# Performance work log

Measured on AMD Instinct MI355X. Metric: run time of the kernel, lower is better.

The kernel has to match this reference:

```python
import jax, jax.numpy as jnp
import numpy as np

B, C_IN, H, W = 8, 32, 64, 64
C = 64  # num_channels


def setup_inputs() -> dict:
    key = jax.random.key(0)
    ks = jax.random.split(key, 9)
    s_in = 1.0 / np.sqrt(C_IN)
    s_c = 1.0 / np.sqrt(C)
    return {
        "x": jax.random.normal(ks[0], (B, C_IN, H, W), dtype=jnp.float32),
        "wq": jax.random.uniform(ks[1], (C, C_IN), jnp.float32, -s_in, s_in),
        "bq": jax.random.uniform(ks[2], (C,), jnp.float32, -s_in, s_in),
        "wk": jax.random.uniform(ks[3], (C, C_IN), jnp.float32, -s_in, s_in),
        "bk": jax.random.uniform(ks[4], (C,), jnp.float32, -s_in, s_in),
        "wv": jax.random.uniform(ks[5], (C, C_IN), jnp.float32, -s_in, s_in),
        "bv": jax.random.uniform(ks[6], (C,), jnp.float32, -s_in, s_in),
        "wo": jax.random.uniform(ks[7], (C_IN, C), jnp.float32, -s_c, s_c),
        "bo": jax.random.uniform(ks[8], (C_IN,), jnp.float32, -s_c, s_c),
    }


def reference(x, wq, bq, wk, bk, wv, bv, wo, bo):
    b, c_in, h, w = x.shape
    n = h * w
    # 1x1 convs == per-pixel linear projections; produce (B, N, C) directly
    q = (jnp.einsum('bchw,oc->bhwo', x, wq) + bq).reshape(b, n, -1)
    k = (jnp.einsum('bchw,oc->bhwo', x, wk) + bk).reshape(b, n, -1)
    v = (jnp.einsum('bchw,oc->bhwo', x, wv) + bv).reshape(b, n, -1)
    # unscaled attention over spatial positions (no 1/sqrt(d) in original)
    scores = jnp.einsum('bnc,bmc->bnm', q, k)  # (B, N, N)
    attn = jax.nn.softmax(scores, axis=-1)
    out = jnp.einsum('bnm,bmc->bnc', attn, v)  # (B, N, C)
    out = out.reshape(b, h, w, -1)
    out = jnp.einsum('bhwc,oc->bohw', out, wo) + bo[None, :, None, None]
    return out + x
```

## Files before the change

### kernel.cpp

```cpp
#include <hip/hip_runtime.h>
#include <hip/hip_bf16.h>

#define CIN    32
#define NPIX   4096
#define DIM    64
#define LOG2E  1.4426950408889634f

#if __has_builtin(__builtin_amdgcn_exp2f)
#define EXP2(x) __builtin_amdgcn_exp2f(x)
#else
#define EXP2(x) exp2f(x)
#endif

typedef float  f32x4  __attribute__((ext_vector_type(4)));
typedef float  f32x16 __attribute__((ext_vector_type(16)));
typedef short  s16x8  __attribute__((ext_vector_type(8)));

#define ZERO16 {0.f,0.f,0.f,0.f,0.f,0.f,0.f,0.f,0.f,0.f,0.f,0.f,0.f,0.f,0.f,0.f}

__device__ __forceinline__ f32x16 mfma32(s16x8 a, s16x8 b, f32x16 c) {
    return __builtin_amdgcn_mfma_f32_32x32x16_bf16(a, b, c, 0, 0, 0);
}


__global__ __launch_bounds__(256) void qkv_proj(
    const float* __restrict__ x,
    const float* __restrict__ wq, const float* __restrict__ bq,
    const float* __restrict__ wk, const float* __restrict__ bk,
    const float* __restrict__ wv, const float* __restrict__ bv,
    __hip_bfloat16* __restrict__ qb, __hip_bfloat16* __restrict__ kb,
    __hip_bfloat16* __restrict__ vb)
{
    __shared__ float Xs[CIN][64];
    __shared__ float wT[3][CIN][DIM];

    const int tid = threadIdx.x;
    const int b   = blockIdx.y;
    const int bx  = blockIdx.x;
    const int n0  = bx * 64;

    for (int i = tid; i < 3 * CIN * DIM; i += 256) {
        int m = i >> 11, r = i & 2047, c = r >> 6, o = r & 63;
        const float* wsrc = (m == 0) ? wq : (m == 1) ? wk : wv;
        float wv0 = wsrc[o * CIN + c];
        wT[m][c][o] = (m == 0) ? wv0 * LOG2E : wv0;
    }
    for (int i = tid * 4; i < CIN * 64; i += 1024) {
        int c = i >> 6, p = i & 63;
        *(f32x4*)&Xs[c][p] = *(const f32x4*)&x[((size_t)b * CIN + c) * NPIX + n0 + p];
    }
    __syncthreads();

    const int w    = tid >> 6;
    const int lane = tid & 63;
    const int l16  = lane >> 2;
    const int quad = lane & 3;

    const int T  = bx * 4 + w;
    const int px = T * 16 + l16;

    float aq[2][8], ak[2][8];
    #pragma unroll
    for (int kb2 = 0; kb2 < 2; kb2++) {
        f32x4 bq0 = *(const f32x4*)&bq[kb2 * 32 + quad * 8];
        f32x4 bq1 = *(const f32x4*)&bq[kb2 * 32 + quad * 8 + 4];
        f32x4 bk0 = *(const f32x4*)&bk[kb2 * 32 + quad * 8];
        f32x4 bk1 = *(const f32x4*)&bk[kb2 * 32 + quad * 8 + 4];
        #pragma unroll
        for (int j = 0; j < 4; j++) {
            aq[kb2][j] = bq0[j] * LOG2E; aq[kb2][j + 4] = bq1[j] * LOG2E;
            ak[kb2][j] = bk0[j];         ak[kb2][j + 4] = bk1[j];
        }
    }
    #pragma unroll 8
    for (int c = 0; c < CIN; c++) {
        const float xc = Xs[c][w * 16 + l16];
        #pragma unroll
        for (int kb2 = 0; kb2 < 2; kb2++) {
            f32x4 q0 = *(const f32x4*)&wT[0][c][kb2 * 32 + quad * 8];
            f32x4 q1 = *(const f32x4*)&wT[0][c][kb2 * 32 + quad * 8 + 4];
            f32x4 k0 = *(const f32x4*)&wT[1][c][kb2 * 32 + quad * 8];
            f32x4 k1 = *(const f32x4*)&wT[1][c][kb2 * 32 + quad * 8 + 4];
            #pragma unroll
            for (int j = 0; j < 4; j++) {
                aq[kb2][j]     += xc * q0[j];
                aq[kb2][j + 4] += xc * q1[j];
                ak[kb2][j]     += xc * k0[j];
                ak[kb2][j + 4] += xc * k1[j];
            }
        }
    }
    {
        const int s   = px >> 5;
        const int key = px & 31;
        #pragma unroll
        for (int kb2 = 0; kb2 < 2; kb2++) {
            union { s16x8 v; __hip_bfloat16 h[8]; } pq, pk;
            #pragma unroll
            for (int j = 0; j < 8; j++) {
                pq.h[j] = __float2bfloat16(aq[kb2][j]);
                pk.h[j] = __float2bfloat16(ak[kb2][j]);
            }
            *(s16x8*)(qb + ((size_t)b * NPIX + px) * DIM + kb2 * 32 + quad * 8) = pq.v;
            const int kt = kb2 * 2 + (quad >> 1);
            const int h  = quad & 1;
            const size_t koff = (size_t)b * 262144
                + ((size_t)(s * 4 + kt) * 64 + h * 32 + key) * 8;
            *(s16x8*)(kb + koff) = pk.v;
        }
    }

    const int ch = w * 16 + l16;
    float av[2][8];
    {
        const float bvc = bv[ch];
        #pragma unroll
        for (int kh = 0; kh < 2; kh++)
            #pragma unroll
            for (int j = 0; j < 8; j++) av[kh][j] = bvc;
    }
    #pragma unroll 8
    for (int c = 0; c < CIN; c++) {
        const float wvc = wT[2][c][ch];
        f32x4 x0 = *(const f32x4*)&Xs[c][quad * 8];
        f32x4 x1 = *(const f32x4*)&Xs[c][quad * 8 + 4];
        f32x4 x2 = *(const f32x4*)&Xs[c][32 + quad * 8];
        f32x4 x3 = *(const f32x4*)&Xs[c][32 + quad * 8 + 4];
        #pragma unroll
        for (int j = 0; j < 4; j++) {
            av[0][j]     += x0[j] * wvc;
            av[0][j + 4] += x1[j] * wvc;
            av[1][j]     += x2[j] * wvc;
            av[1][j + 4] += x3[j] * wvc;
        }
    }
    #pragma unroll
    for (int kh = 0; kh < 2; kh++) {
        const int s = bx * 2 + kh;
        #pragma unroll
        for (int h = 0; h < 2; h++) {
            union { unsigned long long u; __hip_bfloat16 hh[4]; } pv;
            #pragma unroll
            for (int j = 0; j < 4; j++) pv.hh[j] = __float2bfloat16(av[kh][h * 4 + j]);
            const size_t voff = (size_t)b * 262144
                + (size_t)(s * 4 + (ch >> 5) * 2 + (quad >> 1)) * 512
                + (size_t)(h * 32 + (ch & 31)) * 8
                + 4 * (quad & 1);
            *(unsigned long long*)(vb + voff) = pv.u;
        }
    }
}

__global__ __launch_bounds__(512, 2) void attn_fused(
    const __hip_bfloat16* __restrict__ qb,
    const __hip_bfloat16* __restrict__ kbf,
    const __hip_bfloat16* __restrict__ vbf,
    const float* __restrict__ wo, const float* __restrict__ bo,
    const float* __restrict__ x, float* __restrict__ y)
{
    __shared__ __align__(16) char  sm[2][8][4096];
    __shared__ __align__(16) float REDx[4][64][33];
    __shared__ float LRED2[4][32];

    const int tid  = threadIdx.x;
    const int w    = tid >> 6;
    const int g    = w >> 1;
    const int h    = w & 1;
    const int lane = tid & 63;
    const int q    = lane & 31;
    const int hl   = lane >> 5;
    const int b    = blockIdx.x;
    const int row0 = blockIdx.y * 128 + g * 32;

    s16x8 qf[4];
    #pragma unroll
    for (int kt = 0; kt < 4; kt++)
        qf[kt] = *(const s16x8*)(qb + ((size_t)b * NPIX + row0 + q) * DIM
                                 + kt * 16 + hl * 8);

    f32x16 o0 = ZERO16, o1 = ZERO16;
    float lsacc = 0.f;

    const char* stbase = ((w >> 2) ? (const char*)vbf : (const char*)kbf)
                       + (size_t)b * 524288
                       + (size_t)((w >> 1) & 1) * 262144
                       + (size_t)(w & 1) * 4096
                       + (size_t)lane * 16;
    char* std0 = &sm[0][w][lane * 16];
    char* std1 = &sm[1][w][lane * 16];

    #pragma unroll
    for (int i = 0; i < 4; i++)
        *(f32x4*)(std0 + i * 1024) = *(const f32x4*)(stbase + i * 1024);
    __syncthreads();

    int cur = 0;
    for (int p = 0; p < 32; ++p) {
        const size_t srcoff = (size_t)((p < 31) ? p + 1 : 31) * 8192;
        f32x4 r0 = *(const f32x4*)(stbase + srcoff);
        f32x4 r1 = *(const f32x4*)(stbase + srcoff + 1024);
        f32x4 r2 = *(const f32x4*)(stbase + srcoff + 2048);
        f32x4 r3 = *(const f32x4*)(stbase + srcoff + 3072);

        const char* K0 = sm[cur][h * 2 + 0];
        const char* K1 = sm[cur][h * 2 + 1];
        const char* V0 = sm[cur][4 + h * 2 + 0];
        const char* V1 = sm[cur][4 + h * 2 + 1];
        s16x8 kf0[4], kf1[4], vv0[4], vv1[4];
        #pragma unroll
        for (int i = 0; i < 4; i++) {
            kf0[i] = *(const s16x8*)(K0 + i * 1024 + lane * 16);
            kf1[i] = *(const s16x8*)(K1 + i * 1024 + lane * 16);
            vv0[i] = *(const s16x8*)(V0 + i * 1024 + lane * 16);
            vv1[i] = *(const s16x8*)(V1 + i * 1024 + lane * 16);
        }

        __builtin_amdgcn_s_setprio(1);
        f32x16 s0 = ZERO16, s1 = ZERO16;
        s0 = mfma32(kf0[0], qf[0], s0);
        s1 = mfma32(kf1[0], qf[0], s1);
        s0 = mfma32(kf0[1], qf[1], s0);
        s1 = mfma32(kf1[1], qf[1], s1);
        s0 = mfma32(kf0[2], qf[2], s0);
        s1 = mfma32(kf1[2], qf[2], s1);
        s0 = mfma32(kf0[3], qf[3], s0);
        s1 = mfma32(kf1[3], qf[3], s1);
        __builtin_amdgcn_s_setprio(0);

        union { s16x8 v; __hip_bfloat16 h8[8]; } p00, p01, p10, p11;
        #pragma unroll
        for (int r = 0; r < 16; r++) { s0[r] = EXP2(s0[r]); lsacc += s0[r]; }
        #pragma unroll
        for (int j = 0; j < 8; j++) {
            p00.h8[j] = __float2bfloat16(s0[j]);
            p01.h8[j] = __float2bfloat16(s0[8 + j]);
        }
        #pragma unroll
        for (int r = 0; r < 16; r++) { s1[r] = EXP2(s1[r]); lsacc += s1[r]; }
        #pragma unroll
        for (int j = 0; j < 8; j++) {
            p10.h8[j] = __float2bfloat16(s1[j]);
            p11.h8[j] = __float2bfloat16(s1[8 + j]);
        }

        __builtin_amdgcn_s_setprio(1);
        o0 = mfma32(vv0[0], p00.v, o0);
        o1 = mfma32(vv0[2], p00.v, o1);
        o0 = mfma32(vv0[1], p01.v, o0);
        o1 = mfma32(vv0[3], p01.v, o1);
        o0 = mfma32(vv1[0], p10.v, o0);
        o1 = mfma32(vv1[2], p10.v, o1);
        o0 = mfma32(vv1[1], p11.v, o0);
        o1 = mfma32(vv1[3], p11.v, o1);
        __builtin_amdgcn_s_setprio(0);

        char* dst = cur ? std0 : std1;
        *(f32x4*)(dst)        = r0;
        *(f32x4*)(dst + 1024) = r1;
        *(f32x4*)(dst + 2048) = r2;
        *(f32x4*)(dst + 3072) = r3;
        __syncthreads();
        cur ^= 1;
    }

    lsacc += __shfl_xor(lsacc, 32, 64);

    if (h == 1) {
        #pragma unroll
        for (int i = 0; i < 16; i++) {
            const int rr = (i & 3) + 8 * (i >> 2) + 4 * hl;
            REDx[g][rr][q]      = o0[i];
            REDx[g][32 + rr][q] = o1[i];
        }
        if (hl == 0) LRED2[g][q] = lsacc;
    }
    __syncthreads();

    if (h == 0) {
        const float lsum = lsacc + LRED2[g][q];
        #pragma unroll
        for (int i = 0; i < 16; i++) {
            const int rr = (i & 3) + 8 * (i >> 2) + 4 * hl;
            o0[i] += REDx[g][rr][q];
            o1[i] += REDx[g][32 + rr][q];
        }
        const float inv = 1.0f / lsum;

        s16x8 pbo[4];
        #pragma unroll
        for (int gg = 0; gg < 4; gg++) {
            union { s16x8 v; __hip_bfloat16 h8[8]; } pk;
            #pragma unroll
            for (int j = 0; j < 8; j++) {
                const float vv = (gg < 2) ? o0[(gg & 1) * 8 + j] : o1[(gg & 1) * 8 + j];
                pk.h8[j] = __float2bfloat16(vv * inv);
            }
            pbo[gg] = pk.v;
        }

        s16x8 aw[4];
        #pragma unroll
        for (int gg = 0; gg < 4; gg++) {
            f32x4 w0 = *(const f32x4*)(wo + (size_t)q * DIM + gg * 16 + hl * 4);
            f32x4 w1 = *(const f32x4*)(wo + (size_t)q * DIM + gg * 16 + 8 + hl * 4);
            union { s16x8 v; __hip_bfloat16 h8[8]; } wf;
            #pragma unroll
            for (int j = 0; j < 4; j++) {
                wf.h8[j]     = __float2bfloat16(w0[j]);
                wf.h8[4 + j] = __float2bfloat16(w1[j]);
            }
            aw[gg] = wf.v;
        }

        f32x16 d = ZERO16;
        #pragma unroll
        for (int gg = 0; gg < 4; gg++)
            d = mfma32(aw[gg], pbo[gg], d);

        #pragma unroll
        for (int i = 0; i < 16; i++) {
            const int out = (i & 3) + 8 * (i >> 2) + 4 * hl;
            const int row = row0 + q;
            const size_t xi = ((size_t)b * CIN + out) * NPIX + row;
            y[xi] = d[i] + bo[out] + x[xi];
        }
    }
}

extern "C" void kernel_launch(void* const* d_in, const int* in_sizes, int n_in,
                              void* d_out, int out_size, void* d_ws, size_t ws_size,
                              hipStream_t stream)
{
    const float* x  = (const float*)d_in[0];
    const float* wq = (const float*)d_in[1];
    const float* bq = (const float*)d_in[2];
    const float* wk = (const float*)d_in[3];
    const float* bk = (const float*)d_in[4];
    const float* wv = (const float*)d_in[5];
    const float* bv = (const float*)d_in[6];
    const float* wo = (const float*)d_in[7];
    const float* bo = (const float*)d_in[8];
    float* y = (float*)d_out;

    char* ws = (char*)d_ws;
    __hip_bfloat16* qb = (__hip_bfloat16*)(ws);
    __hip_bfloat16* kb = (__hip_bfloat16*)(ws + (4u << 20));
    __hip_bfloat16* vb = (__hip_bfloat16*)(ws + (8u << 20));

    qkv_proj<<<dim3(64, 8), dim3(256), 0, stream>>>(x, wq, bq, wk, bk, wv, bv, qb, kb, vb);
    attn_fused<<<dim3(8, 32), dim3(512), 0, stream>>>(qb, kb, vb, wo, bo, x, y);
}
```

Measured before the change: 127.6 us.

## Software-pipeline PV MFMAs one tile behind QK and exp in attention loop

```diff
diff --git a/kernel.cpp b/kernel.cpp
--- a/kernel.cpp
+++ b/kernel.cpp
@@ -194,25 +194,40 @@
         *(f32x4*)(std0 + i * 1024) = *(const f32x4*)(stbase + i * 1024);
     __syncthreads();
 
-    int cur = 0;
-    for (int p = 0; p < 32; ++p) {
+    s16x8 vvA[8], vvB[8], pA[4], pB[4];
+
+    auto phase = [&](int p, int cur,
+                     s16x8 (&vvP)[8], s16x8 (&pP)[4],
+                     s16x8 (&vvO)[8], s16x8 (&pO)[4], bool do_pv) {
+        const char* K0 = sm[cur][h * 2 + 0];
+        const char* K1 = sm[cur][h * 2 + 1];
+        const char* V0 = sm[cur][4 + h * 2 + 0];
+        const char* V1 = sm[cur][4 + h * 2 + 1];
+        s16x8 kf0[4], kf1[4];
+        #pragma unroll
+        for (int i = 0; i < 4; i++) {
+            kf0[i]     = *(const s16x8*)(K0 + i * 1024 + lane * 16);
+            kf1[i]     = *(const s16x8*)(K1 + i * 1024 + lane * 16);
+            vvO[i]     = *(const s16x8*)(V0 + i * 1024 + lane * 16);
+            vvO[4 + i] = *(const s16x8*)(V1 + i * 1024 + lane * 16);
+        }
         const size_t srcoff = (size_t)((p < 31) ? p + 1 : 31) * 8192;
         f32x4 r0 = *(const f32x4*)(stbase + srcoff);
         f32x4 r1 = *(const f32x4*)(stbase + srcoff + 1024);
         f32x4 r2 = *(const f32x4*)(stbase + srcoff + 2048);
         f32x4 r3 = *(const f32x4*)(stbase + srcoff + 3072);
 
-        const char* K0 = sm[cur][h * 2 + 0];
-        const char* K1 = sm[cur][h * 2 + 1];
-        const char* V0 = sm[cur][4 + h * 2 + 0];
-        const char* V1 = sm[cur][4 + h * 2 + 1];
-        s16x8 kf0[4], kf1[4], vv0[4], vv1[4];
-        #pragma unroll
-        for (int i = 0; i < 4; i++) {
-            kf0[i] = *(const s16x8*)(K0 + i * 1024 + lane * 16);
-            kf1[i] = *(const s16x8*)(K1 + i * 1024 + lane * 16);
-            vv0[i] = *(const s16x8*)(V0 + i * 1024 + lane * 16);
-            vv1[i] = *(const s16x8*)(V1 + i * 1024 + lane * 16);
+        if (do_pv) {
+            __builtin_amdgcn_s_setprio(1);
+            o0 = mfma32(vvP[0], pP[0], o0);
+            o1 = mfma32(vvP[2], pP[0], o1);
+            o0 = mfma32(vvP[1], pP[1], o0);
+            o1 = mfma32(vvP[3], pP[1], o1);
+            o0 = mfma32(vvP[4], pP[2], o0);
+            o1 = mfma32(vvP[6], pP[2], o1);
+            o0 = mfma32(vvP[5], pP[3], o0);
+            o1 = mfma32(vvP[7], pP[3], o1);
+            __builtin_amdgcn_s_setprio(0);
         }
 
         __builtin_amdgcn_s_setprio(1);
@@ -227,32 +242,24 @@
         s1 = mfma32(kf1[3], qf[3], s1);
         __builtin_amdgcn_s_setprio(0);
 
-        union { s16x8 v; __hip_bfloat16 h8[8]; } p00, p01, p10, p11;
-        #pragma unroll
-        for (int r = 0; r < 16; r++) { s0[r] = EXP2(s0[r]); lsacc += s0[r]; }
+        union { s16x8 v; __hip_bfloat16 h8[8]; } u0, u1, u2, u3;
         #pragma unroll
         for (int j = 0; j < 8; j++) {
-            p00.h8[j] = __float2bfloat16(s0[j]);
-            p01.h8[j] = __float2bfloat16(s0[8 + j]);
-        }
-        #pragma unroll
-        for (int r = 0; r < 16; r++) { s1[r] = EXP2(s1[r]); lsacc += s1[r]; }
+            float e0 = EXP2(s0[j]);
+            float e1 = EXP2(s0[8 + j]);
+            lsacc += e0 + e1;
+            u0.h8[j] = __float2bfloat16(e0);
+            u1.h8[j] = __float2bfloat16(e1);
+        }
         #pragma unroll
         for (int j = 0; j < 8; j++) {
-            p10.h8[j] = __float2bfloat16(s1[j]);
-            p11.h8[j] = __float2bfloat16(s1[8 + j]);
-        }
-
-        __builtin_amdgcn_s_setprio(1);
-        o0 = mfma32(vv0[0], p00.v, o0);
-        o1 = mfma32(vv0[2], p00.v, o1);
-        o0 = mfma32(vv0[1], p01.v, o0);
-        o1 = mfma32(vv0[3], p01.v, o1);
-        o0 = mfma32(vv1[0], p10.v, o0);
-        o1 = mfma32(vv1[2], p10.v, o1);
-        o0 = mfma32(vv1[1], p11.v, o0);
-        o1 = mfma32(vv1[3], p11.v, o1);
-        __builtin_amdgcn_s_setprio(0);
+            float e0 = EXP2(s1[j]);
+            float e1 = EXP2(s1[8 + j]);
+            lsacc += e0 + e1;
+            u2.h8[j] = __float2bfloat16(e0);
+            u3.h8[j] = __float2bfloat16(e1);
+        }
+        pO[0] = u0.v; pO[1] = u1.v; pO[2] = u2.v; pO[3] = u3.v;
 
         char* dst = cur ? std0 : std1;
         *(f32x4*)(dst)        = r0;
@@ -260,8 +267,24 @@
         *(f32x4*)(dst + 2048) = r2;
         *(f32x4*)(dst + 3072) = r3;
         __syncthreads();
-        cur ^= 1;
-    }
+    };
+
+    phase(0, 0, vvB, pB, vvA, pA, false);
+    for (int it = 0; it < 15; ++it) {
+        phase(2 * it + 1, 1, vvA, pA, vvB, pB, true);
+        phase(2 * it + 2, 0, vvB, pB, vvA, pA, true);
+    }
+    phase(31, 1, vvA, pA, vvB, pB, true);
+    __builtin_amdgcn_s_setprio(1);
+    o0 = mfma32(vvB[0], pB[0], o0);
+    o1 = mfma32(vvB[2], pB[0], o1);
+    o0 = mfma32(vvB[1], pB[1], o0);
+    o1 = mfma32(vvB[3], pB[1], o1);
+    o0 = mfma32(vvB[4], pB[2], o0);
+    o1 = mfma32(vvB[6], pB[2], o1);
+    o0 = mfma32(vvB[5], pB[3], o0);
+    o1 = mfma32(vvB[7], pB[3], o1);
+    __builtin_amdgcn_s_setprio(0);
 
     lsacc += __shfl_xor(lsacc, 32, 64);
 
@@ -292,8 +315,8 @@
             union { s16x8 v; __hip_bfloat16 h8[8]; } pk;
             #pragma unroll
             for (int j = 0; j < 8; j++) {
-                const float vv = (gg < 2) ? o0[(gg & 1) * 8 + j] : o1[(gg & 1) * 8 + j];
-                pk.h8[j] = __float2bfloat16(vv * inv);
+                const float vv2 = (gg < 2) ? o0[(gg & 1) * 8 + j] : o1[(gg & 1) * 8 + j];
+                pk.h8[j] = __float2bfloat16(vv2 * inv);
             }
             pbo[gg] = pk.v;
         }
```

After: 127.0 us. Within noise of the previous version (-0.5%).

## Compute QKV projection with split-bf16 MFMA instead of scalar FMA

Applied to the files above, without the earlier changes.

```diff
diff --git a/kernel.cpp b/kernel.cpp
--- a/kernel.cpp
+++ b/kernel.cpp
@@ -31,124 +31,119 @@
     __hip_bfloat16* __restrict__ qb, __hip_bfloat16* __restrict__ kb,
     __hip_bfloat16* __restrict__ vb)
 {
-    __shared__ float Xs[CIN][64];
-    __shared__ float wT[3][CIN][DIM];
-
-    const int tid = threadIdx.x;
-    const int b   = blockIdx.y;
-    const int bx  = blockIdx.x;
-    const int n0  = bx * 64;
-
-    for (int i = tid; i < 3 * CIN * DIM; i += 256) {
-        int m = i >> 11, r = i & 2047, c = r >> 6, o = r & 63;
-        const float* wsrc = (m == 0) ? wq : (m == 1) ? wk : wv;
-        float wv0 = wsrc[o * CIN + c];
-        wT[m][c][o] = (m == 0) ? wv0 * LOG2E : wv0;
+    const int tid  = threadIdx.x;
+    const int wid  = tid >> 6;
+    const int lane = tid & 63;
+    const int l31  = lane & 31;
+    const int hl   = lane >> 5;
+    const int b    = blockIdx.y;
+    const int bx   = blockIdx.x;
+    const int s    = bx * 4 + wid;
+    const int px   = s * 32 + l31;
+
+    s16x8 xhi[2], xlo[2];
+    #pragma unroll
+    for (int kt = 0; kt < 2; kt++) {
+        union { s16x8 v; __hip_bfloat16 h8[8]; } uh, ul;
+        #pragma unroll
+        for (int j = 0; j < 8; j++) {
+            const int c = kt * 16 + hl * 8 + j;
+            const float xv = x[((size_t)b * CIN + c) * NPIX + px];
+            const __hip_bfloat16 hi = __float2bfloat16(xv);
+            uh.h8[j] = hi;
+            ul.h8[j] = __float2bfloat16(xv - __bfloat162float(hi));
+        }
+        xhi[kt] = uh.v; xlo[kt] = ul.v;
     }
-    for (int i = tid * 4; i < CIN * 64; i += 1024) {
-        int c = i >> 6, p = i & 63;
-        *(f32x4*)&Xs[c][p] = *(const f32x4*)&x[((size_t)b * CIN + c) * NPIX + n0 + p];
-    }
-    __syncthreads();
-
-    const int w    = tid >> 6;
-    const int lane = tid & 63;
-    const int l16  = lane >> 2;
-    const int quad = lane & 3;
-
-    const int T  = bx * 4 + w;
-    const int px = T * 16 + l16;
-
-    float aq[2][8], ak[2][8];
-    #pragma unroll
-    for (int kb2 = 0; kb2 < 2; kb2++) {
-        f32x4 bq0 = *(const f32x4*)&bq[kb2 * 32 + quad * 8];
-        f32x4 bq1 = *(const f32x4*)&bq[kb2 * 32 + quad * 8 + 4];
-        f32x4 bk0 = *(const f32x4*)&bk[kb2 * 32 + quad * 8];
-        f32x4 bk1 = *(const f32x4*)&bk[kb2 * 32 + quad * 8 + 4];
-        #pragma unroll
-        for (int j = 0; j < 4; j++) {
-            aq[kb2][j] = bq0[j] * LOG2E; aq[kb2][j + 4] = bq1[j] * LOG2E;
-            ak[kb2][j] = bk0[j];         ak[kb2][j + 4] = bk1[j];
-        }
-    }
-    #pragma unroll 8
-    for (int c = 0; c < CIN; c++) {
-        const float xc = Xs[c][w * 16 + l16];
-        #pragma unroll
-        for (int kb2 = 0; kb2 < 2; kb2++) {
-            f32x4 q0 = *(const f32x4*)&wT[0][c][kb2 * 32 + quad * 8];
-            f32x4 q1 = *(const f32x4*)&wT[0][c][kb2 * 32 + quad * 8 + 4];
-            f32x4 k0 = *(const f32x4*)&wT[1][c][kb2 * 32 + quad * 8];
-            f32x4 k1 = *(const f32x4*)&wT[1][c][kb2 * 32 + quad * 8 + 4];
-            #pragma unroll
-            for (int j = 0; j < 4; j++) {
-                aq[kb2][j]     += xc * q0[j];
-                aq[kb2][j + 4] += xc * q1[j];
-                ak[kb2][j]     += xc * k0[j];
-                ak[kb2][j + 4] += xc * k1[j];
-            }
-        }
-    }
-    {
-        const int s   = px >> 5;
-        const int key = px & 31;
-        #pragma unroll
-        for (int kb2 = 0; kb2 < 2; kb2++) {
-            union { s16x8 v; __hip_bfloat16 h[8]; } pq, pk;
-            #pragma unroll
-            for (int j = 0; j < 8; j++) {
-                pq.h[j] = __float2bfloat16(aq[kb2][j]);
-                pk.h[j] = __float2bfloat16(ak[kb2][j]);
-            }
-            *(s16x8*)(qb + ((size_t)b * NPIX + px) * DIM + kb2 * 32 + quad * 8) = pq.v;
-            const int kt = kb2 * 2 + (quad >> 1);
-            const int h  = quad & 1;
-            const size_t koff = (size_t)b * 262144
-                + ((size_t)(s * 4 + kt) * 64 + h * 32 + key) * 8;
-            *(s16x8*)(kb + koff) = pk.v;
-        }
-    }
-
-    const int ch = w * 16 + l16;
-    float av[2][8];
-    {
-        const float bvc = bv[ch];
-        #pragma unroll
-        for (int kh = 0; kh < 2; kh++)
-            #pragma unroll
-            for (int j = 0; j < 8; j++) av[kh][j] = bvc;
-    }
-    #pragma unroll 8
-    for (int c = 0; c < CIN; c++) {
-        const float wvc = wT[2][c][ch];
-        f32x4 x0 = *(const f32x4*)&Xs[c][quad * 8];
-        f32x4 x1 = *(const f32x4*)&Xs[c][quad * 8 + 4];
-        f32x4 x2 = *(const f32x4*)&Xs[c][32 + quad * 8];
-        f32x4 x3 = *(const f32x4*)&Xs[c][32 + quad * 8 + 4];
-        #pragma unroll
-        for (int j = 0; j < 4; j++) {
-            av[0][j]     += x0[j] * wvc;
-            av[0][j + 4] += x1[j] * wvc;
-            av[1][j]     += x2[j] * wvc;
-            av[1][j + 4] += x3[j] * wvc;
-        }
-    }
-    #pragma unroll
-    for (int kh = 0; kh < 2; kh++) {
-        const int s = bx * 2 + kh;
-        #pragma unroll
-        for (int h = 0; h < 2; h++) {
-            union { unsigned long long u; __hip_bfloat16 hh[4]; } pv;
-            #pragma unroll
-            for (int j = 0; j < 4; j++) pv.hh[j] = __float2bfloat16(av[kh][h * 4 + j]);
-            const size_t voff = (size_t)b * 262144
-                + (size_t)(s * 4 + (ch >> 5) * 2 + (quad >> 1)) * 512
-                + (size_t)(h * 32 + (ch & 31)) * 8
-                + 4 * (quad & 1);
-            *(unsigned long long*)(vb + voff) = pv.u;
-        }
-    }
+
+    auto do_mat = [&](const float* __restrict__ W, const float* __restrict__ B,
+                      int which) {
+        const float scale = (which == 0) ? LOG2E : 1.0f;
+        s16x8 whi[2][2], wlo[2][2];
+        #pragma unroll
+        for (int t = 0; t < 2; t++)
+            #pragma unroll
+            for (int kt = 0; kt < 2; kt++) {
+                const float* wp = W + (size_t)(t * 32 + l31) * CIN + kt * 16 + hl * 8;
+                f32x4 a0 = *(const f32x4*)wp;
+                f32x4 a1 = *(const f32x4*)(wp + 4);
+                union { s16x8 v; __hip_bfloat16 h8[8]; } uh, ul;
+                #pragma unroll
+                for (int j = 0; j < 4; j++) {
+                    const float v0 = a0[j] * scale, v1 = a1[j] * scale;
+                    const __hip_bfloat16 h0 = __float2bfloat16(v0);
+                    const __hip_bfloat16 h1 = __float2bfloat16(v1);
+                    uh.h8[j] = h0; uh.h8[4 + j] = h1;
+                    ul.h8[j]     = __float2bfloat16(v0 - __bfloat162float(h0));
+                    ul.h8[4 + j] = __float2bfloat16(v1 - __bfloat162float(h1));
+                }
+                whi[t][kt] = uh.v; wlo[t][kt] = ul.v;
+            }
+
+        f32x16 acc0 = ZERO16, acc1 = ZERO16;
+        if (which < 2) {
+            #pragma unroll
+            for (int kt = 0; kt < 2; kt++) {
+                acc0 = mfma32(whi[0][kt], xhi[kt], acc0);
+                acc1 = mfma32(whi[1][kt], xhi[kt], acc1);
+                acc0 = mfma32(whi[0][kt], xlo[kt], acc0);
+                acc1 = mfma32(whi[1][kt], xlo[kt], acc1);
+                acc0 = mfma32(wlo[0][kt], xhi[kt], acc0);
+                acc1 = mfma32(wlo[1][kt], xhi[kt], acc1);
+            }
+            #pragma unroll
+            for (int t = 0; t < 2; t++) {
+                const f32x16 acc = t ? acc1 : acc0;
+                #pragma unroll
+                for (int ig = 0; ig < 4; ig++) {
+                    f32x4 b4 = *(const f32x4*)(B + t * 32 + ig * 8 + hl * 4);
+                    union { unsigned long long u; __hip_bfloat16 h4[4]; } st;
+                    #pragma unroll
+                    for (int r = 0; r < 4; r++)
+                        st.h4[r] = __float2bfloat16(acc[ig * 4 + r] + b4[r] * scale);
+                    if (which == 0) {
+                        const size_t off = ((size_t)b * NPIX + px) * DIM
+                                         + t * 32 + ig * 8 + hl * 4;
+                        *(unsigned long long*)(qb + off) = st.u;
+                    } else {
+                        const size_t off = (size_t)b * 262144
+                            + ((size_t)(s * 4 + 2 * t + (ig >> 1)) * 64
+                               + (ig & 1) * 32 + l31) * 8 + 4 * hl;
+                        *(unsigned long long*)(kb + off) = st.u;
+                    }
+                }
+            }
+        } else {
+            #pragma unroll
+            for (int kt = 0; kt < 2; kt++) {
+                acc0 = mfma32(xhi[kt], whi[0][kt], acc0);
+                acc1 = mfma32(xhi[kt], whi[1][kt], acc1);
+                acc0 = mfma32(xlo[kt], whi[0][kt], acc0);
+                acc1 = mfma32(xlo[kt], whi[1][kt], acc1);
+                acc0 = mfma32(xhi[kt], wlo[0][kt], acc0);
+                acc1 = mfma32(xhi[kt], wlo[1][kt], acc1);
+            }
+            #pragma unroll
+            for (int t = 0; t < 2; t++) {
+                const f32x16 acc = t ? acc1 : acc0;
+                const float bvv = B[t * 32 + l31];
+                #pragma unroll
+                for (int m = 0; m < 2; m++) {
+                    union { s16x8 v; __hip_bfloat16 h8[8]; } st;
+                    #pragma unroll
+                    for (int e = 0; e < 8; e++)
+                        st.h8[e] = __float2bfloat16(acc[m * 8 + e] + bvv);
+                    const size_t off = (size_t)b * 262144
+                        + ((size_t)(s * 4 + 2 * t + m) * 64 + hl * 32 + l31) * 8;
+                    *(s16x8*)(vb + off) = st.v;
+                }
+            }
+        }
+    };
+
+    do_mat(wq, bq, 0);
+    do_mat(wk, bk, 1);
+    do_mat(wv, bv, 2);
 }
 
 __global__ __launch_bounds__(512, 2) void attn_fused(
@@ -292,8 +287,8 @@
             union { s16x8 v; __hip_bfloat16 h8[8]; } pk;
             #pragma unroll
             for (int j = 0; j < 8; j++) {
-                const float vv = (gg < 2) ? o0[(gg & 1) * 8 + j] : o1[(gg & 1) * 8 + j];
-                pk.h8[j] = __float2bfloat16(vv * inv);
+                const float vv2 = (gg < 2) ? o0[(gg & 1) * 8 + j] : o1[(gg & 1) * 8 + j];
+                pk.h8[j] = __float2bfloat16(vv2 * inv);
             }
             pbo[gg] = pk.v;
         }
@@ -347,6 +342,6 @@
     __hip_bfloat16* kb = (__hip_bfloat16*)(ws + (4u << 20));
     __hip_bfloat16* vb = (__hip_bfloat16*)(ws + (8u << 20));
 
-    qkv_proj<<<dim3(64, 8), dim3(256), 0, stream>>>(x, wq, bq, wk, bk, wv, bv, qb, kb, vb);
+    qkv_proj<<<dim3(32, 8), dim3(256), 0, stream>>>(x, wq, bq, wk, bk, wv, bv, qb, kb, vb);
     attn_fused<<<dim3(8, 32), dim3(512), 0, stream>>>(qb, kb, vb, wo, bo, x, y);
 }
```

Result: faster. 118.2 us (-7.4%).
